# Kernel optimization log

Hardware: AMD Instinct MI355X
Metric: run time of the kernel (lower is better)

Reference implementation:

```python
import jax, jax.numpy as jnp
import numpy as np

# Broyden low-rank inverse-Jacobian matvecs. Us: [b,d,e,T], VTs: [b,T,d,e], x: [b,d,e].
# Unwritten history slots are zero, so using the full buffers equals torch's :nstep slicing.

def _matvec(Us, VTs, x):
    VTx = jnp.einsum('btde,bde->bt', VTs, x)
    return -x + jnp.einsum('bdet,bt->bde', Us, VTx)

def _rmatvec(Us, VTs, x):
    xTU = jnp.einsum('bde,bdet->bt', x, Us)
    return -x + jnp.einsum('bt,btde->bde', xTU, VTs)

def broyden(g, x0, threshold, eps):
    """Faithful port of broyden(..., ls=False): line search returns s=1 always."""
    B, D, E = x0.shape
    T = min(threshold, 27)
    gx0 = g(x0)
    init_obj = jnp.linalg.norm(gx0)
    protect = init_obj * (1e6 * E)  # protect_thres = 1e6 * n_elem
    Us0 = jnp.zeros((B, D, E, T), x0.dtype)
    VTs0 = jnp.zeros((B, T, D, E), x0.dtype)

    def cond(s):
        nstep, x, gx, upd, Us, VTs, obj, low, lx, lg = s
        return (obj >= eps) & (nstep < threshold) & (obj <= protect)

    def body(s):
        nstep, x, gx, upd, Us, VTs, obj, low, lx, lg = s
        x_new = x + upd                     # step size s = 1 (ls off)
        gx_new = g(x_new)
        dx, dg = upd, gx_new - gx
        nstep = nstep + 1
        obj_new = jnp.linalg.norm(gx_new)
        better = obj_new < low
        low = jnp.where(better, obj_new, low)
        lx = jnp.where(better, x_new, lx)
        lg = jnp.where(better, gx_new, lg)
        # Broyden rank-1 update of the inverse-Jacobian history
        vT = _rmatvec(Us, VTs, dx)
        denom = jnp.einsum('bde,bde->b', vT, dg)
        u = (dx - _matvec(Us, VTs, dg)) / denom[:, None, None]
        vT = jnp.where(jnp.isnan(vT), 0.0, vT)
        u = jnp.where(jnp.isnan(u), 0.0, u)
        Us = Us.at[:, :, :, (nstep - 1) % T].set(u)
        VTs = VTs.at[:, (nstep - 1) % T].set(vT)
        upd = -_matvec(Us, VTs, gx_new)
        return (nstep, x_new, gx_new, upd, Us, VTs, obj_new, low, lx, lg)

    s0 = (jnp.int32(0), x0, gx0, gx0, Us0, VTs0, init_obj, init_obj, x0, gx0)
    s = jax.lax.while_loop(cond, body, s0)
    return s[8], jnp.linalg.norm(s[9])  # lowest_xest, ||lowest_gx||


def f_layer(z, x, W, U, b):
    return jnp.tanh(z @ W + x @ U + b)


def setup_inputs() -> dict:
    key = jax.random.key(0)
    k1, k2, k3, k4 = jax.random.split(key, 4)
    B, D = 256, 2048
    x = jax.random.normal(k1, (B, D), jnp.float32)
    initial_point = jnp.zeros((B, D), jnp.float32)
    W = jax.random.normal(k2, (D, D), jnp.float32) * (0.4 / np.sqrt(D))  # contractive in z
    U = jax.random.normal(k3, (D, D), jnp.float32) * (1.0 / np.sqrt(D))
    b = jax.random.normal(k4, (D,), jnp.float32) * 0.01
    return {"x": x, "initial_point": initial_point, "W": W, "U": U, "b": b}


def reference(x, initial_point, W, U, b):
    MAX_ITER = 12  # kwargs['max_iter']
    B = x.shape[0]

    def g(z_flat):  # broyd_output_test: f(z, x) - z, flattened to [B, D, 1]
        z = z_flat[..., 0]
        return (f_layer(z, x, W, U, b) - z)[..., None]

    z0 = initial_point.reshape(B, -1, 1)
    out_x, _ = broyden(g, z0, MAX_ITER, 1e-8)
    z = f_layer(out_x[..., 0].reshape(x.shape), x, W, U, b)
    return z
```

## Files before the change

### kernel.cpp

```cpp
#include <hip/hip_runtime.h>
#include <math.h>


#define DD 2048
#define KA 4096
#define KW 2048
#define BB 256
#define BD (BB * DD)
#define TT 12
#define NKS 8

#define ST_S   0
#define ST_A   169
#define ST_B   325
#define ST_PHI 481
#define ST_XI  494
#define ST_XSN 507
#define ST_SZ  1024

typedef unsigned short ushort_t;
typedef _Float16 half_t;
typedef __attribute__((ext_vector_type(8))) short short8;
typedef __attribute__((ext_vector_type(4))) float floatx4;
typedef __attribute__((ext_vector_type(4))) _Float16 half4;

__device__ __forceinline__ ushort_t f2bf(float f) {
    unsigned int u = __float_as_uint(f);
    unsigned int r = (u + 0x7FFFu + ((u >> 16) & 1u)) >> 16;
    return (ushort_t)r;
}
__device__ __forceinline__ float bf2f(ushort_t h) {
    return __uint_as_float(((unsigned int)h) << 16);
}
__device__ __forceinline__ void gload_lds16(const void* g, void* l) {
    __builtin_amdgcn_global_load_lds(
        (const __attribute__((address_space(1))) unsigned int*)g,
        (__attribute__((address_space(3))) unsigned int*)l, 16, 0, 0);
}
__device__ __forceinline__ float wave_red(float v) {
#pragma unroll
    for (int off = 32; off > 0; off >>= 1) v += __shfl_down(v, off, 64);
    return v;
}

__global__ __launch_bounds__(256)
void convert_w(const float* __restrict__ W, const float* __restrict__ U,
               ushort_t* __restrict__ Wt, ushort_t* __restrict__ Ut) {
    const float* src = blockIdx.z ? U : W;
    ushort_t* dst = blockIdx.z ? Ut : Wt;
    __shared__ ushort_t Hs[64][65];
    const int tid = threadIdx.x;
    const int k0 = blockIdx.y * 64, n0 = blockIdx.x * 64;
    const int r = tid >> 4, c4 = (tid & 15) * 4;
#pragma unroll
    for (int i = 0; i < 4; ++i) {
        int kr = r + i * 16;
        float4 w = *(const float4*)(src + (size_t)(k0 + kr) * DD + n0 + c4);
        Hs[kr][c4 + 0] = f2bf(w.x); Hs[kr][c4 + 1] = f2bf(w.y);
        Hs[kr][c4 + 2] = f2bf(w.z); Hs[kr][c4 + 3] = f2bf(w.w);
    }
    __syncthreads();
#pragma unroll
    for (int i = 0; i < 4; ++i) {
        int nr = r + i * 16;
        ushort4 hv = { Hs[c4+0][nr], Hs[c4+1][nr], Hs[c4+2][nr], Hs[c4+3][nr] };
        *(ushort4*)(dst + (size_t)(n0 + nr) * KW + (size_t)(k0 + c4)) = hv;
    }
}

__global__ void init_misc(const float* __restrict__ xin, ushort_t* __restrict__ Axx,
                          float* __restrict__ stbase) {
    const int i4 = blockIdx.x * 256 + threadIdx.x;
    const int idx = i4 * 4;
    const int m = idx >> 11, col = idx & 2047;
    float4 xv = ((const float4*)xin)[i4];
    float a[4] = {xv.x, xv.y, xv.z, xv.w};
    ushort_t hh[4], ll[4];
#pragma unroll
    for (int j = 0; j < 4; ++j) { hh[j] = f2bf(a[j]); ll[j] = f2bf(a[j] - bf2f(hh[j])); }
    ushort4 h = {hh[0],hh[1],hh[2],hh[3]}, l = {ll[0],ll[1],ll[2],ll[3]};
    size_t ab = (size_t)m * KA + col;
    *(ushort4*)(Axx + ab) = h; *(ushort4*)(Axx + ab + DD) = l;
    if (i4 < 65544) {
        float4 z = {0.f, 0.f, 0.f, 0.f};
        ((float4*)stbase)[i4] = z;
    }
}

template<int LDA, int KSLICE, int NIT, int BMOD, typename YT>
__global__ __launch_bounds__(512)
void gemm_t(const ushort_t* __restrict__ A, const ushort_t* __restrict__ Bt,
            YT* __restrict__ y) {
    __shared__ ushort_t As[2][256 * 64];
    __shared__ ushort_t Bs[2][64 * 64];
    const int tid = threadIdx.x;
    const int lane = tid & 63, w = tid >> 6;
    const int bn = blockIdx.x * 64;
    const int ks = blockIdx.y;
    const int waveM = w >> 1, waveN = w & 1;

    const int srow = tid >> 3;
    const int sg = (tid & 7) ^ (srow & 7);
    const ushort_t* Ag = A  + (size_t)srow * LDA + ks * KSLICE + sg * 8;
    const ushort_t* Bg = Bt + (size_t)(bn + srow) * KW + (ks & BMOD) * KSLICE + sg * 8;
    const size_t rs64 = (size_t)64 * LDA;

    const int q = lane >> 4, rl = lane & 15;
    int offA[2][4], offB[2][2];
#pragma unroll
    for (int kk = 0; kk < 2; ++kk) {
        int j = kk * 4 + q;
#pragma unroll
        for (int mi = 0; mi < 4; ++mi) {
            int m = waveM * 64 + mi * 16 + rl;
            offA[kk][mi] = (m * 8 + (j ^ (m & 7))) * 8;
        }
#pragma unroll
        for (int ni = 0; ni < 2; ++ni) {
            int n = waveN * 32 + ni * 16 + rl;
            offB[kk][ni] = (n * 8 + (j ^ (n & 7))) * 8;
        }
    }

    floatx4 acc[4][2];
#pragma unroll
    for (int mi = 0; mi < 4; ++mi)
#pragma unroll
        for (int ni = 0; ni < 2; ++ni) acc[mi][ni] = (floatx4){0.f,0.f,0.f,0.f};

    gload_lds16(Ag,            As[0] + tid * 8);
    gload_lds16(Ag + rs64,     As[0] + (512 + tid) * 8);
    gload_lds16(Ag + 2 * rs64, As[0] + (1024 + tid) * 8);
    gload_lds16(Ag + 3 * rs64, As[0] + (1536 + tid) * 8);
    gload_lds16(Bg,            Bs[0] + tid * 8);
    Ag += 64; Bg += 64;
    __syncthreads();

    for (int it = 0; it < NIT; ++it) {
        const int cur = it & 1, nxt = cur ^ 1;
        if (it + 1 < NIT) {
            gload_lds16(Ag,            As[nxt] + tid * 8);
            gload_lds16(Ag + rs64,     As[nxt] + (512 + tid) * 8);
            gload_lds16(Ag + 2 * rs64, As[nxt] + (1024 + tid) * 8);
            gload_lds16(Ag + 3 * rs64, As[nxt] + (1536 + tid) * 8);
            gload_lds16(Bg,            Bs[nxt] + tid * 8);
            Ag += 64; Bg += 64;
        }
        const ushort_t* Ab = As[cur];
        const ushort_t* Bb = Bs[cur];
#pragma unroll
        for (int kk = 0; kk < 2; ++kk) {
            short8 b0 = *(const short8*)(Bb + offB[kk][0]);
            short8 b1 = *(const short8*)(Bb + offB[kk][1]);
#pragma unroll
            for (int mi = 0; mi < 4; ++mi) {
                short8 a = *(const short8*)(Ab + offA[kk][mi]);
                acc[mi][0] = __builtin_amdgcn_mfma_f32_16x16x32_bf16(a, b0, acc[mi][0], 0, 0, 0);
                acc[mi][1] = __builtin_amdgcn_mfma_f32_16x16x32_bf16(a, b1, acc[mi][1], 0, 0, 0);
            }
        }
        __syncthreads();
    }

    YT* yp = y + (size_t)ks * BD;
    const int mb = waveM * 64 + q * 4;
    const int nb = bn + waveN * 32 + rl;
#pragma unroll
    for (int mi = 0; mi < 4; ++mi)
#pragma unroll
        for (int r = 0; r < 4; ++r) {
            yp[(size_t)(mb + mi * 16 + r) * DD + nb]      = (YT)acc[mi][0][r];
            yp[(size_t)(mb + mi * 16 + r) * DD + nb + 16] = (YT)acc[mi][1][r];
        }
}

__global__ __launch_bounds__(512)
void epi0(const float* __restrict__ y, const float* __restrict__ bias,
          float* __restrict__ c, ushort_t* __restrict__ gxp,
          ushort_t* __restrict__ Azz, float* __restrict__ state,
          float* __restrict__ scal) {
    __shared__ float red[8];
    const int tid = threadIdx.x;
    const int b = blockIdx.x;
    const int col = tid * 4;
    const size_t base = (size_t)b * DD + col;

    float4 cc = *(const float4*)(bias + col);
#pragma unroll
    for (int s = 0; s < NKS; ++s) {
        float4 v = *(const float4*)(y + (size_t)s * BD + base);
        cc.x += v.x; cc.y += v.y; cc.z += v.z; cc.w += v.w;
    }
    *(float4*)(c + base) = cc;
    float4 g = { tanhf(cc.x), tanhf(cc.y), tanhf(cc.z), tanhf(cc.w) };
    ushort4 gs = { f2bf(g.x), f2bf(g.y), f2bf(g.z), f2bf(g.w) };
    *(ushort4*)(gxp + base) = gs;
    *(ushort4*)(Azz + base) = gs;

    float pd = g.x*g.x + g.y*g.y + g.z*g.z + g.w*g.w;
    pd = wave_red(pd);
    if ((tid & 63) == 0) red[tid >> 6] = pd;
    __syncthreads();
    if (tid == 0) {
        float t = 0.f;
#pragma unroll
        for (int w2 = 0; w2 < 8; ++w2) t += red[w2];
        float* stb = state + (size_t)b * ST_SZ;
        stb[ST_S + 0]   = t;
        stb[ST_PHI + 0] = 1.f;
        stb[ST_XI + 0]  = 1.f;
        atomicAdd(&scal[0], t);
    }
}

__global__ __launch_bounds__(512)
void broyden_gram(const half_t* __restrict__ yh, const float* __restrict__ c,
                  ushort_t* __restrict__ gxp, ushort_t* __restrict__ Azz,
                  float* __restrict__ state, float* __restrict__ scal, int k)
{
    __shared__ float red[8][16];
    __shared__ float dots[14];
    __shared__ float Sl[169], Al[156], Bl[156], PHl[13], XIl[13];
    __shared__ float newA[14], newB[14], nphi[14];
    __shared__ double dyv[13], dxtu[12], dvdg[12], dcgx[13], dden[1];
    const int tid = threadIdx.x;
    const int lane = tid & 63, w = tid >> 6;
    const int b = blockIdx.x;
    const int p = k - 1;
    float* stb = state + (size_t)b * ST_SZ;

    for (int i = tid; i < 169; i += 512) Sl[i] = stb[ST_S + i];
    for (int i = tid; i < 156; i += 512) { Al[i] = stb[ST_A + i]; Bl[i] = stb[ST_B + i]; }
    if (tid < 13) { PHl[tid] = stb[ST_PHI + tid]; XIl[tid] = stb[ST_XI + tid]; }

    const int col = tid * 4;
    const size_t base = (size_t)b * DD + col;
    float4 pre = *(const float4*)(c + base);
#pragma unroll
    for (int s = 0; s < NKS; ++s) {
        half4 v = *(const half4*)(yh + (size_t)s * BD + base);
        pre.x += (float)v.x; pre.y += (float)v.y;
        pre.z += (float)v.z; pre.w += (float)v.w;
    }

    float4 G[12];
#pragma unroll
    for (int j = 0; j < 12; ++j)
        if (j < k) {
            ushort4 gu = *(const ushort4*)(gxp + (size_t)j * BD + base);
            G[j] = (float4){ bf2f(gu.x), bf2f(gu.y), bf2f(gu.z), bf2f(gu.w) };
        }

    __syncthreads();

    float4 x = {0.f, 0.f, 0.f, 0.f};
#pragma unroll
    for (int j = 0; j < 12; ++j)
        if (j < k) {
            float xc = XIl[j];
            x.x = fmaf(xc, G[j].x, x.x); x.y = fmaf(xc, G[j].y, x.y);
            x.z = fmaf(xc, G[j].z, x.z); x.w = fmaf(xc, G[j].w, x.w);
        }
    float4 gk = { tanhf(pre.x) - x.x, tanhf(pre.y) - x.y,
                  tanhf(pre.z) - x.z, tanhf(pre.w) - x.w };

#pragma unroll
    for (int j = 0; j < 12; ++j)
        if (j < k) {
            float pd = G[j].x*gk.x + G[j].y*gk.y + G[j].z*gk.z + G[j].w*gk.w;
            pd = wave_red(pd);
            if (lane == 0) red[w][j] = pd;
        }
    {
        float pdk = gk.x*gk.x + gk.y*gk.y + gk.z*gk.z + gk.w*gk.w;
        pdk = wave_red(pdk);
        if (lane == 0) red[w][k] = pdk;
    }
    __syncthreads();
    if (tid <= k) {
        float s = 0.f;
#pragma unroll
        for (int w2 = 0; w2 < 8; ++w2) s += red[w2][tid];
        dots[tid] = s;
        if (tid == k) atomicAdd(&scal[k], s);
    }
    __syncthreads();

    if (tid < k) {
        double s = 0.0;
        for (int j = 0; j < k; ++j) s += (double)Sl[tid*13 + j] * (double)PHl[j];
        dyv[tid] = s;
    }
    __syncthreads();
    if (tid < p) {
        double sx = 0.0, sv = 0.0;
        for (int j = 0; j < k; ++j) {
            sx += (double)Al[tid*13 + j] * dyv[j];
            sv += (double)Bl[tid*13 + j] * ((double)dots[j] - (double)Sl[j*13 + (k-1)]);
        }
        dxtu[tid] = sx; dvdg[tid] = sv;
    }
    __syncthreads();
    if (tid < k) {
        double s = -(double)PHl[tid];
        for (int t = 0; t < p; ++t) s += dxtu[t] * (double)Bl[t*13 + tid];
        newB[tid] = (float)s;
    }
    __syncthreads();
    if (tid == 0) {
        double s = 0.0;
        for (int j = 0; j < k; ++j)
            s += (double)newB[j] * ((double)dots[j] - (double)Sl[j*13 + (k-1)]);
        dden[0] = s;
    }
    __syncthreads();
    if (tid <= k) {
        double s = (double)((tid < 13) ? PHl[tid] : 0.f);
        if (tid == k)     s += 1.0;
        if (tid == k - 1) s -= 1.0;
        for (int t = 0; t < p; ++t) s -= dvdg[t] * (double)Al[t*13 + tid];
        newA[tid] = (float)(s / dden[0]);
    }
    if (tid >= 32 && tid < 32 + p) {
        int t = tid - 32;
        double s = 0.0;
        for (int j = 0; j < k; ++j) s += (double)Bl[t*13 + j] * (double)dots[j];
        dcgx[t] = s;
    }
    if (tid == 63) {
        double s = 0.0;
        for (int j = 0; j < k; ++j) s += (double)newB[j] * (double)dots[j];
        dcgx[p] = s;
    }
    __syncthreads();
    if (tid <= k) {
        double s = (tid == k) ? 1.0 : 0.0;
        for (int t = 0; t < p; ++t) s -= dcgx[t] * (double)Al[t*13 + tid];
        s -= dcgx[p] * (double)newA[tid];
        nphi[tid] = (float)s;
    }
    __syncthreads();

    if (tid <= k) {
        stb[ST_S + k*13 + tid] = dots[tid];
        stb[ST_S + tid*13 + k] = dots[tid];
        stb[ST_A + p*13 + tid] = newA[tid];
        stb[ST_PHI + tid] = nphi[tid];
        float xi_old = (tid < 13) ? XIl[tid] : 0.f;
        stb[ST_XI + tid] = xi_old + nphi[tid];
    }
    if (tid < k) stb[ST_B + p*13 + tid] = newB[tid];
    if (tid < 13) stb[ST_XSN + k*13 + tid] = XIl[tid];

    {
        ushort4 gs = { f2bf(gk.x), f2bf(gk.y), f2bf(gk.z), f2bf(gk.w) };
        *(ushort4*)(gxp + (size_t)k * BD + base) = gs;
    }

    if (k < TT) {
        float4 xn = x;
#pragma unroll
        for (int j = 0; j < 12; ++j)
            if (j < k) {
                float fc = nphi[j];
                xn.x = fmaf(fc, G[j].x, xn.x); xn.y = fmaf(fc, G[j].y, xn.y);
                xn.z = fmaf(fc, G[j].z, xn.z); xn.w = fmaf(fc, G[j].w, xn.w);
            }
        float fk = nphi[k];
        xn.x = fmaf(fk, gk.x, xn.x); xn.y = fmaf(fk, gk.y, xn.y);
        xn.z = fmaf(fk, gk.z, xn.z); xn.w = fmaf(fk, gk.w, xn.w);

        ushort4 h = { f2bf(xn.x), f2bf(xn.y), f2bf(xn.z), f2bf(xn.w) };
        *(ushort4*)(Azz + base) = h;
    }
}

__global__ __launch_bounds__(256)
void final_out(const ushort_t* __restrict__ gxp, const float* __restrict__ state,
               const float* __restrict__ scal, float* __restrict__ out) {
    const int i4 = blockIdx.x * 256 + threadIdx.x;
    float best = scal[0];
    int bk = 0;
#pragma unroll
    for (int k = 1; k <= TT; ++k) {
        float o = scal[k];
        if (o < best) { best = o; bk = k; }
    }
    const size_t idx = (size_t)i4 * 4;
    const int m = (int)(idx >> 11);
    const float* cf = state + (size_t)m * ST_SZ + ST_XSN + bk * 13;
    ushort4 gb = *(const ushort4*)(gxp + (size_t)bk * BD + idx);
    float4 r = { bf2f(gb.x), bf2f(gb.y), bf2f(gb.z), bf2f(gb.w) };
    for (int j = 0; j < bk; ++j) {
        float c1 = cf[j];
        ushort4 gu = *(const ushort4*)(gxp + (size_t)j * BD + idx);
        r.x = fmaf(c1, bf2f(gu.x), r.x); r.y = fmaf(c1, bf2f(gu.y), r.y);
        r.z = fmaf(c1, bf2f(gu.z), r.z); r.w = fmaf(c1, bf2f(gu.w), r.w);
    }
    ((float4*)out)[i4] = r;
}

extern "C" void kernel_launch(void* const* d_in, const int* in_sizes, int n_in,
                              void* d_out, int out_size, void* d_ws, size_t ws_size,
                              hipStream_t stream) {
    const float* xin  = (const float*)d_in[0];
    const float* W    = (const float*)d_in[2];
    const float* U    = (const float*)d_in[3];
    const float* bias = (const float*)d_in[4];
    float* out = (float*)d_out;

    float* ws = (float*)d_ws;
    float* c      = ws;
    float* y      = ws + 1 * (size_t)BD;
    ushort_t* gxp = (ushort_t*)(ws + 9 * (size_t)BD);
    ushort_t* Axx = (ushort_t*)(ws + 16 * (size_t)BD);
    ushort_t* Azz = (ushort_t*)(ws + 17 * (size_t)BD);
    ushort_t* Wt  = (ushort_t*)(ws + 18 * (size_t)BD);
    ushort_t* Ut  = (ushort_t*)(ws + 22 * (size_t)BD);
    float* state  = ws + 26 * (size_t)BD;
    float* scal   = state + (size_t)BB * ST_SZ;

    convert_w<<<dim3(32, 32, 2), 256, 0, stream>>>(W, U, Wt, Ut);
    init_misc<<<512, 256, 0, stream>>>(xin, Axx, state);

    dim3 gg(32, NKS);
    gemm_t<4096, 512, 8, 3, float><<<gg, 512, 0, stream>>>(Axx, Ut, y);
    epi0<<<BB, 512, 0, stream>>>(y, bias, c, gxp, Azz, state, scal);

    for (int k = 1; k <= TT; ++k) {
        gemm_t<2048, 256, 4, 7, half_t><<<gg, 512, 0, stream>>>(Azz, Wt, (half_t*)y);
        broyden_gram<<<BB, 512, 0, stream>>>((const half_t*)y, c, gxp, Azz, state, scal, k);
    }

    final_out<<<512, 256, 0, stream>>>(gxp, state, scal, out);
}
```

Measured before the change: 366.5 us.

## Split GEMM M into two 128-row tiles, halve split-K, merge prep kernels

The GEMM block tile shrinks from 256 to 128 rows of M, with a new grid dimension covering the two M tiles. The split-K factor drops from 8 to 4, so each block runs twice as many K iterations and fewer partial outputs are written and later reduced. The two setup kernels (weight transpose/convert and input split/state zeroing) are merged into one launch. Block count stays the same, but each block uses less LDS and does less work per K step. This may change occupancy and latency hiding, and it cuts partial-sum traffic in exchange for a longer serial K loop.

```diff
diff --git a/kernel.cpp b/kernel.cpp
--- a/kernel.cpp
+++ b/kernel.cpp
@@ -8,7 +8,7 @@
 #define BB 256
 #define BD (BB * DD)
 #define TT 12
-#define NKS 8
+#define NKS 4
 
 #define ST_S   0
 #define ST_A   169
@@ -44,46 +44,49 @@
 }
 
 __global__ __launch_bounds__(256)
-void convert_w(const float* __restrict__ W, const float* __restrict__ U,
-               ushort_t* __restrict__ Wt, ushort_t* __restrict__ Ut) {
-    const float* src = blockIdx.z ? U : W;
-    ushort_t* dst = blockIdx.z ? Ut : Wt;
+void prep(const float* __restrict__ W, const float* __restrict__ U,
+          ushort_t* __restrict__ Wt, ushort_t* __restrict__ Ut,
+          const float* __restrict__ xin, ushort_t* __restrict__ Axx,
+          float* __restrict__ stbase) {
     __shared__ ushort_t Hs[64][65];
+    const int bid = blockIdx.x;
     const int tid = threadIdx.x;
-    const int k0 = blockIdx.y * 64, n0 = blockIdx.x * 64;
-    const int r = tid >> 4, c4 = (tid & 15) * 4;
-#pragma unroll
-    for (int i = 0; i < 4; ++i) {
-        int kr = r + i * 16;
-        float4 w = *(const float4*)(src + (size_t)(k0 + kr) * DD + n0 + c4);
-        Hs[kr][c4 + 0] = f2bf(w.x); Hs[kr][c4 + 1] = f2bf(w.y);
-        Hs[kr][c4 + 2] = f2bf(w.z); Hs[kr][c4 + 3] = f2bf(w.w);
-    }
-    __syncthreads();
-#pragma unroll
-    for (int i = 0; i < 4; ++i) {
-        int nr = r + i * 16;
-        ushort4 hv = { Hs[c4+0][nr], Hs[c4+1][nr], Hs[c4+2][nr], Hs[c4+3][nr] };
-        *(ushort4*)(dst + (size_t)(n0 + nr) * KW + (size_t)(k0 + c4)) = hv;
-    }
-}
-
-__global__ void init_misc(const float* __restrict__ xin, ushort_t* __restrict__ Axx,
-                          float* __restrict__ stbase) {
-    const int i4 = blockIdx.x * 256 + threadIdx.x;
-    const int idx = i4 * 4;
-    const int m = idx >> 11, col = idx & 2047;
-    float4 xv = ((const float4*)xin)[i4];
-    float a[4] = {xv.x, xv.y, xv.z, xv.w};
-    ushort_t hh[4], ll[4];
-#pragma unroll
-    for (int j = 0; j < 4; ++j) { hh[j] = f2bf(a[j]); ll[j] = f2bf(a[j] - bf2f(hh[j])); }
-    ushort4 h = {hh[0],hh[1],hh[2],hh[3]}, l = {ll[0],ll[1],ll[2],ll[3]};
-    size_t ab = (size_t)m * KA + col;
-    *(ushort4*)(Axx + ab) = h; *(ushort4*)(Axx + ab + DD) = l;
-    if (i4 < 65544) {
-        float4 z = {0.f, 0.f, 0.f, 0.f};
-        ((float4*)stbase)[i4] = z;
+    if (bid < 2048) {
+        const int bz = bid >> 10, by = (bid >> 5) & 31, bx = bid & 31;
+        const float* src = bz ? U : W;
+        ushort_t* dst = bz ? Ut : Wt;
+        const int k0 = by * 64, n0 = bx * 64;
+        const int r = tid >> 4, c4 = (tid & 15) * 4;
+#pragma unroll
+        for (int i = 0; i < 4; ++i) {
+            int kr = r + i * 16;
+            float4 w = *(const float4*)(src + (size_t)(k0 + kr) * DD + n0 + c4);
+            Hs[kr][c4 + 0] = f2bf(w.x); Hs[kr][c4 + 1] = f2bf(w.y);
+            Hs[kr][c4 + 2] = f2bf(w.z); Hs[kr][c4 + 3] = f2bf(w.w);
+        }
+        __syncthreads();
+#pragma unroll
+        for (int i = 0; i < 4; ++i) {
+            int nr = r + i * 16;
+            ushort4 hv = { Hs[c4+0][nr], Hs[c4+1][nr], Hs[c4+2][nr], Hs[c4+3][nr] };
+            *(ushort4*)(dst + (size_t)(n0 + nr) * KW + (size_t)(k0 + c4)) = hv;
+        }
+    } else {
+        const int i4 = (bid - 2048) * 256 + tid;
+        const int idx = i4 * 4;
+        const int m = idx >> 11, col = idx & 2047;
+        float4 xv = ((const float4*)xin)[i4];
+        float a[4] = {xv.x, xv.y, xv.z, xv.w};
+        ushort_t hh[4], ll[4];
+#pragma unroll
+        for (int j = 0; j < 4; ++j) { hh[j] = f2bf(a[j]); ll[j] = f2bf(a[j] - bf2f(hh[j])); }
+        ushort4 h = {hh[0],hh[1],hh[2],hh[3]}, l = {ll[0],ll[1],ll[2],ll[3]};
+        size_t ab = (size_t)m * KA + col;
+        *(ushort4*)(Axx + ab) = h; *(ushort4*)(Axx + ab + DD) = l;
+        if (i4 < 65544) {
+            float4 z = {0.f, 0.f, 0.f, 0.f};
+            ((float4*)stbase)[i4] = z;
+        }
     }
 }
 
@@ -91,28 +94,29 @@
 __global__ __launch_bounds__(512)
 void gemm_t(const ushort_t* __restrict__ A, const ushort_t* __restrict__ Bt,
             YT* __restrict__ y) {
-    __shared__ ushort_t As[2][256 * 64];
+    __shared__ ushort_t As[2][128 * 64];
     __shared__ ushort_t Bs[2][64 * 64];
     const int tid = threadIdx.x;
     const int lane = tid & 63, w = tid >> 6;
     const int bn = blockIdx.x * 64;
-    const int ks = blockIdx.y;
+    const int mt = blockIdx.y;
+    const int ks = blockIdx.z;
     const int waveM = w >> 1, waveN = w & 1;
 
     const int srow = tid >> 3;
     const int sg = (tid & 7) ^ (srow & 7);
-    const ushort_t* Ag = A  + (size_t)srow * LDA + ks * KSLICE + sg * 8;
+    const ushort_t* Ag = A  + (size_t)(mt * 128 + srow) * LDA + ks * KSLICE + sg * 8;
     const ushort_t* Bg = Bt + (size_t)(bn + srow) * KW + (ks & BMOD) * KSLICE + sg * 8;
     const size_t rs64 = (size_t)64 * LDA;
 
     const int q = lane >> 4, rl = lane & 15;
-    int offA[2][4], offB[2][2];
+    int offA[2][2], offB[2][2];
 #pragma unroll
     for (int kk = 0; kk < 2; ++kk) {
         int j = kk * 4 + q;
 #pragma unroll
-        for (int mi = 0; mi < 4; ++mi) {
-            int m = waveM * 64 + mi * 16 + rl;
+        for (int mi = 0; mi < 2; ++mi) {
+            int m = waveM * 32 + mi * 16 + rl;
             offA[kk][mi] = (m * 8 + (j ^ (m & 7))) * 8;
         }
 #pragma unroll
@@ -122,28 +126,24 @@
         }
     }
 
-    floatx4 acc[4][2];
-#pragma unroll
-    for (int mi = 0; mi < 4; ++mi)
+    floatx4 acc[2][2];
+#pragma unroll
+    for (int mi = 0; mi < 2; ++mi)
 #pragma unroll
         for (int ni = 0; ni < 2; ++ni) acc[mi][ni] = (floatx4){0.f,0.f,0.f,0.f};
 
-    gload_lds16(Ag,            As[0] + tid * 8);
-    gload_lds16(Ag + rs64,     As[0] + (512 + tid) * 8);
-    gload_lds16(Ag + 2 * rs64, As[0] + (1024 + tid) * 8);
-    gload_lds16(Ag + 3 * rs64, As[0] + (1536 + tid) * 8);
-    gload_lds16(Bg,            Bs[0] + tid * 8);
+    gload_lds16(Ag,        As[0] + tid * 8);
+    gload_lds16(Ag + rs64, As[0] + (512 + tid) * 8);
+    gload_lds16(Bg,        Bs[0] + tid * 8);
     Ag += 64; Bg += 64;
     __syncthreads();
 
     for (int it = 0; it < NIT; ++it) {
         const int cur = it & 1, nxt = cur ^ 1;
         if (it + 1 < NIT) {
-            gload_lds16(Ag,            As[nxt] + tid * 8);
-            gload_lds16(Ag + rs64,     As[nxt] + (512 + tid) * 8);
-            gload_lds16(Ag + 2 * rs64, As[nxt] + (1024 + tid) * 8);
-            gload_lds16(Ag + 3 * rs64, As[nxt] + (1536 + tid) * 8);
-            gload_lds16(Bg,            Bs[nxt] + tid * 8);
+            gload_lds16(Ag,        As[nxt] + tid * 8);
+            gload_lds16(Ag + rs64, As[nxt] + (512 + tid) * 8);
+            gload_lds16(Bg,        Bs[nxt] + tid * 8);
             Ag += 64; Bg += 64;
         }
         const ushort_t* Ab = As[cur];
@@ -153,7 +153,7 @@
             short8 b0 = *(const short8*)(Bb + offB[kk][0]);
             short8 b1 = *(const short8*)(Bb + offB[kk][1]);
 #pragma unroll
-            for (int mi = 0; mi < 4; ++mi) {
+            for (int mi = 0; mi < 2; ++mi) {
                 short8 a = *(const short8*)(Ab + offA[kk][mi]);
                 acc[mi][0] = __builtin_amdgcn_mfma_f32_16x16x32_bf16(a, b0, acc[mi][0], 0, 0, 0);
                 acc[mi][1] = __builtin_amdgcn_mfma_f32_16x16x32_bf16(a, b1, acc[mi][1], 0, 0, 0);
@@ -163,10 +163,10 @@
     }
 
     YT* yp = y + (size_t)ks * BD;
-    const int mb = waveM * 64 + q * 4;
+    const int mb = mt * 128 + waveM * 32 + q * 4;
     const int nb = bn + waveN * 32 + rl;
 #pragma unroll
-    for (int mi = 0; mi < 4; ++mi)
+    for (int mi = 0; mi < 2; ++mi)
 #pragma unroll
         for (int r = 0; r < 4; ++r) {
             yp[(size_t)(mb + mi * 16 + r) * DD + nb]      = (YT)acc[mi][0][r];
@@ -420,15 +420,14 @@
     float* state  = ws + 26 * (size_t)BD;
     float* scal   = state + (size_t)BB * ST_SZ;
 
-    convert_w<<<dim3(32, 32, 2), 256, 0, stream>>>(W, U, Wt, Ut);
-    init_misc<<<512, 256, 0, stream>>>(xin, Axx, state);
-
-    dim3 gg(32, NKS);
-    gemm_t<4096, 512, 8, 3, float><<<gg, 512, 0, stream>>>(Axx, Ut, y);
+    prep<<<2560, 256, 0, stream>>>(W, U, Wt, Ut, xin, Axx, state);
+
+    dim3 gg(32, 2, NKS);
+    gemm_t<4096, 1024, 16, 1, float><<<gg, 512, 0, stream>>>(Axx, Ut, y);
     epi0<<<BB, 512, 0, stream>>>(y, bias, c, gxp, Azz, state, scal);
 
     for (int k = 1; k <= TT; ++k) {
-        gemm_t<2048, 256, 4, 7, half_t><<<gg, 512, 0, stream>>>(Azz, Wt, (half_t*)y);
+        gemm_t<2048, 512, 8, 3, half_t><<<gg, 512, 0, stream>>>(Azz, Wt, (half_t*)y);
         broyden_gram<<<BB, 512, 0, stream>>>((const half_t*)y, c, gxp, Azz, state, scal, k);
     }
 
```

New measurement: 349.0 us. 1.05x faster.
